# Kernel tuning notes

Measured on AMD Instinct MI355X. Metric: run time of the kernel, lower is better.

Reference implementation:

```python
import jax, jax.numpy as jnp
import numpy as np

SCALE = 8      # scale_factor from map_to_mat_info
PATCH = 32     # up_delta - low_delta + 1 == right_delta - left_delta + 1 (uniform interior patches)


def setup_inputs() -> dict:
    key = jax.random.key(0)
    mat_h, mat_w = 160, 160
    H = (mat_h - 1) * SCALE + PATCH  # 1304: deltas (0,31,0,31) -> no border clipping
    W = (mat_w - 1) * SCALE + PATCH
    x = jax.random.normal(key, (1, 3, H, W), dtype=jnp.float32)
    rgb_weight = jnp.array([0.299, 0.587, 0.114], dtype=jnp.float32).reshape(1, 3, 1, 1)
    return {"x": x, "rgb_weight": rgb_weight, "mat_h": mat_h, "mat_w": mat_w}


def reference(x, rgb_weight, mat_h, mat_w):
    P = PATCH
    # RGB -> grayscale (convert_gray branch for in_channels == 3)
    gray = jnp.sum(x * rgb_weight, axis=1)[0]  # (H, W)
    # Gather all overlapping PxP patches at stride SCALE -> (mat_h, mat_w, P, P)
    rows = (jnp.arange(mat_h) * SCALE)[:, None] + jnp.arange(P)[None, :]  # (mat_h, P)
    cols = (jnp.arange(mat_w) * SCALE)[:, None] + jnp.arange(P)[None, :]  # (mat_w, P)
    p = gray[rows.reshape(-1)].reshape(mat_h, P, -1)              # (mat_h, P, W)
    p = p[:, :, cols.reshape(-1)].reshape(mat_h, P, mat_w, P)     # (mat_h, P, mat_w, P)
    patches = jnp.transpose(p, (0, 2, 1, 3))                      # (mat_h, mat_w, P, P)
    # torch.rfft(signal_ndim=2, onesided=False) == full 2D FFT; power = re^2 + im^2
    F = jnp.fft.fft2(patches)
    log_power = jnp.log(F.real * F.real + F.imag * F.imag + 1.0)
    # High-frequency region sums (h == w == P, static)
    lo = P // 2 - P // 4 - 1   # 7
    up = P // 2 + P // 4       # 24
    r1 = jnp.sum(log_power[..., lo:up + 1, :], axis=(-2, -1))
    r2 = jnp.sum(log_power[..., up + 1:, lo:up + 1], axis=(-2, -1))
    r3 = jnp.sum(log_power[..., :lo, lo:up + 1], axis=(-2, -1))
    mat = (r1 + r2 + r3)[None, None]  # (1, 1, mat_h, mat_w)
    return mat / jnp.max(mat)
```

## Files before the change

kernel.cpp:

```cpp
#include <hip/hip_runtime.h>
#include <math.h>

#define SCALE 8
#define PSZ 32

__device__ constexpr float C32[16] = {
     1.000000000000000f,  0.980785280403230f,  0.923879532511287f,  0.831469612302545f,
     0.707106781186548f,  0.555570233019602f,  0.382683432365090f,  0.195090322016128f,
     0.000000000000000f, -0.195090322016128f, -0.382683432365090f, -0.555570233019602f,
    -0.707106781186548f, -0.831469612302545f, -0.923879532511287f, -0.980785280403230f };
__device__ constexpr float S32[16] = {
     0.000000000000000f,  0.195090322016128f,  0.382683432365090f,  0.555570233019602f,
     0.707106781186548f,  0.831469612302545f,  0.923879532511287f,  0.980785280403230f,
     1.000000000000000f,  0.980785280403230f,  0.923879532511287f,  0.831469612302545f,
     0.707106781186548f,  0.555570233019602f,  0.382683432365090f,  0.195090322016128f };

__device__ __forceinline__ constexpr int brev4(int i) {
    return ((i & 1) << 3) | ((i & 2) << 1) | ((i & 4) >> 1) | ((i & 8) >> 3);
}

__device__ __forceinline__ void fft16(float re[16], float im[16]) {
#pragma unroll
    for (int i = 0; i < 16; ++i) {
        const int j = brev4(i);
        if (j > i) {
            float t = re[i]; re[i] = re[j]; re[j] = t;
            t = im[i]; im[i] = im[j]; im[j] = t;
        }
    }
#pragma unroll
    for (int s = 1; s <= 4; ++s) {
        const int m = 1 << s;
        const int h = m >> 1;
        const int tstep = 32 >> s;
#pragma unroll
        for (int k = 0; k < 16; k += m) {
#pragma unroll
            for (int j = 0; j < h; ++j) {
                const float wr = C32[j * tstep];
                const float wi = -S32[j * tstep];
                const int a = k + j;
                const int b = k + j + h;
                const float tr = wr * re[b] - wi * im[b];
                const float ti = wr * im[b] + wi * re[b];
                re[b] = re[a] - tr; im[b] = im[a] - ti;
                re[a] = re[a] + tr; im[a] = im[a] + ti;
            }
        }
    }
}

__device__ __forceinline__ unsigned pack_bf2(float hi, float lo) {
    const unsigned uh = __float_as_uint(hi) + 0x8000u;
    const unsigned ul = __float_as_uint(lo) + 0x8000u;
    return (uh & 0xFFFF0000u) | (ul >> 16);
}
__device__ __forceinline__ float bf_hi(unsigned u) { return __uint_as_float(u & 0xFFFF0000u); }
__device__ __forceinline__ float bf_lo(unsigned u) { return __uint_as_float(u << 16); }

__global__ __launch_bounds__(256) void gray_kernel(
        const float* __restrict__ x, const float* __restrict__ w,
        float* __restrict__ g, int n4, long long HW) {
    const int i = blockIdx.x * 256 + threadIdx.x;
    if (i >= n4) return;
    const float w0 = w[0], w1 = w[1], w2 = w[2];
    const float4 a = reinterpret_cast<const float4*>(x)[i];
    const float4 b = reinterpret_cast<const float4*>(x + HW)[i];
    const float4 c = reinterpret_cast<const float4*>(x + 2 * HW)[i];
    float4 o;
    o.x = w0 * a.x + w1 * b.x + w2 * c.x;
    o.y = w0 * a.y + w1 * b.y + w2 * c.y;
    o.z = w0 * a.z + w1 * b.z + w2 * c.z;
    o.w = w0 * a.w + w1 * b.w + w2 * c.w;
    reinterpret_cast<float4*>(g)[i] = o;
}

template <bool GRAY_PRE>
__global__ __launch_bounds__(128) void hfdft_patch_kernel(
        const float* __restrict__ x, const float* __restrict__ w,
        float* __restrict__ out, int H, int W, int mat_h, int mat_w) {
    __shared__ unsigned cb[4 * 528];
    __shared__ float red[8];

    const int tid = threadIdx.x;
    const int h = tid >> 6;
    const int lane = tid & 63;
    const int total = mat_h * mat_w;
    const long long HW = (long long)H * W;
    const int Pbase = blockIdx.x * 4;

    {
        const int g = lane >> 5, r = lane & 31;
        int pA = Pbase + 2 * g;
        if (pA > total - 1) pA = total - 1;
        int pB = pA + 1; if (pB > total - 1) pB = total - 1;
        const int phA = pA / mat_w, pwA = pA % mat_w;
        const int phB = pB / mat_w, pwB = pB % mat_w;
        const bool adj = (phA == phB) && (pwB == pwA + 1);
        const int baseA = (phA * SCALE + r) * W + pwA * SCALE;
        const int baseB = (phB * SCALE + r) * W + pwB * SCALE;

        float ar[32], br[32];
        if (GRAY_PRE && adj) {
            float win[40];
            const float4* g4 = reinterpret_cast<const float4*>(x + baseA);
#pragma unroll
            for (int q = 0; q < 10; ++q) {
                const float4 v = g4[q];
                win[4 * q + 0] = v.x; win[4 * q + 1] = v.y;
                win[4 * q + 2] = v.z; win[4 * q + 3] = v.w;
            }
#pragma unroll
            for (int i = 0; i < 32; ++i) { ar[i] = win[i]; br[i] = win[i + 8]; }
        } else if (GRAY_PRE) {
#pragma unroll
            for (int i = 0; i < 32; ++i) { ar[i] = x[baseA + i]; br[i] = x[baseB + i]; }
        } else {
            const float w0 = w[0], w1 = w[1], w2 = w[2];
#pragma unroll
            for (int i = 0; i < 32; ++i) {
                ar[i] = w0 * x[baseA + i] + w1 * x[HW + baseA + i] + w2 * x[2 * HW + baseA + i];
                br[i] = w0 * x[baseB + i] + w1 * x[HW + baseB + i] + w2 * x[2 * HW + baseB + i];
            }
        }

        float fr[16], fi[16];
        if (h == 0) {
#pragma unroll
            for (int i = 0; i < 16; ++i) {
                fr[i] = ar[i] + ar[i + 16];
                fi[i] = br[i] + br[i + 16];
            }
        } else {
#pragma unroll
            for (int i = 0; i < 16; ++i) {
                const float dre = ar[i] - ar[i + 16];
                const float dim = br[i] - br[i + 16];
                fr[i] = dre * C32[i] + dim * S32[i];
                fi[i] = dim * C32[i] - dre * S32[i];
            }
        }

        fft16(fr, fi);

        unsigned* cbA = cb + (2 * g) * 528;
        unsigned* cbB = cbA + 528;
        if (h == 0) {
            cbA[r] = pack_bf2(fr[0], fr[8]);
            cbB[r] = pack_bf2(fi[0], fi[8]);
#pragma unroll
            for (int k2 = 1; k2 <= 7; ++k2) {
                const int e2 = 16 - k2;
                const float far_ = 0.5f * (fr[k2] + fr[e2]);
                const float fai_ = 0.5f * (fi[k2] - fi[e2]);
                const float fbr_ = 0.5f * (fi[k2] + fi[e2]);
                const float fbi_ = 0.5f * (fr[e2] - fr[k2]);
                cbA[(2 * k2) * 33 + r] = pack_bf2(far_, fai_);
                cbB[(2 * k2) * 33 + r] = pack_bf2(fbr_, fbi_);
            }
        } else {
#pragma unroll
            for (int k2 = 0; k2 <= 7; ++k2) {
                const int o2 = 15 - k2;
                const float far_ = 0.5f * (fr[k2] + fr[o2]);
                const float fai_ = 0.5f * (fi[k2] - fi[o2]);
                const float fbr_ = 0.5f * (fi[k2] + fi[o2]);
                const float fbi_ = 0.5f * (fr[o2] - fr[k2]);
                cbA[(2 * k2 + 1) * 33 + r] = pack_bf2(far_, fai_);
                cbB[(2 * k2 + 1) * 33 + r] = pack_bf2(fbr_, fbi_);
            }
        }
    }

    __syncthreads();

    {
        const int pl = lane >> 4, slot = lane & 15;
        int p = Pbase + pl;
        if (p > total - 1) p = total - 1;
        const unsigned* cbp = cb + pl * 528 + slot * 33;

        float fr[16], fi[16];
        if (h == 0) {
#pragma unroll
            for (int i = 0; i < 16; ++i) {
                const unsigned u0 = cbp[i], u1 = cbp[i + 16];
                fr[i] = bf_hi(u0) + bf_hi(u1);
                fi[i] = bf_lo(u0) + bf_lo(u1);
            }
        } else {
#pragma unroll
            for (int i = 0; i < 16; ++i) {
                const unsigned u0 = cbp[i], u1 = cbp[i + 16];
                const float dre = bf_hi(u0) - bf_hi(u1);
                const float dim = bf_lo(u0) - bf_lo(u1);
                fr[i] = dre * C32[i] + dim * S32[i];
                fi[i] = dim * C32[i] - dre * S32[i];
            }
        }

        fft16(fr, fi);

        float s0 = 0.0f, s1 = 0.0f;
        if (slot == 0) {
            if (h == 0) {
#pragma unroll
                for (int k2 = 0; k2 <= 8; ++k2) {
                    const int kr = 2 * k2;
                    const int b = (k2 == 0) ? 0 : 16 - k2;
                    const float g0r = 0.5f * (fr[k2] + fr[b]);
                    const float g0i = 0.5f * (fi[k2] - fi[b]);
                    const float g1r = 0.5f * (fi[k2] + fi[b]);
                    const float g1i = 0.5f * (fr[b] - fr[k2]);
                    const float w0c = (kr >= 7 ? 1.0f : 0.0f) + ((kr >= 8 && kr <= 15) ? 1.0f : 0.0f);
                    const float w16c = 1.0f + ((kr >= 1 && kr <= 15) ? 1.0f : 0.0f);
                    if (w0c > 0.0f)
                        s0 = fmaf(w0c, __logf(g0r * g0r + g0i * g0i + 1.0f), s0);
                    s1 = fmaf(w16c, __logf(g1r * g1r + g1i * g1i + 1.0f), s1);
                }
            } else {
#pragma unroll
                for (int k2 = 0; k2 <= 7; ++k2) {
                    const int kr = 2 * k2 + 1;
                    const int b = 15 - k2;
                    const float g0r = 0.5f * (fr[k2] + fr[b]);
                    const float g0i = 0.5f * (fi[k2] - fi[b]);
                    const float g1r = 0.5f * (fi[k2] + fi[b]);
                    const float g1i = 0.5f * (fr[b] - fr[k2]);
                    const float w0c = (kr >= 7 ? 1.0f : 0.0f) + ((kr >= 8 && kr <= 15) ? 1.0f : 0.0f);
                    const float w16c = 2.0f;
                    if (w0c > 0.0f)
                        s0 = fmaf(w0c, __logf(g0r * g0r + g0i * g0i + 1.0f), s0);
                    s1 = fmaf(w16c, __logf(g1r * g1r + g1i * g1i + 1.0f), s1);
                }
            }
        } else {
            const float b1f = (slot >= 7) ? 1.0f : 0.0f;
            const float m1f = (slot >= 8) ? 1.0f : 0.0f;
            if (h == 0) {
#pragma unroll
                for (int k2 = 0; k2 < 16; ++k2) {
                    const int kr = 2 * k2;
                    const float lp = __logf(fr[k2] * fr[k2] + fi[k2] * fi[k2] + 1.0f);
                    const float wgt = (kr >= 8 && kr <= 24) ? 2.0f : (b1f + m1f);
                    if (k2 & 1) s1 = fmaf(wgt, lp, s1);
                    else        s0 = fmaf(wgt, lp, s0);
                }
            } else {
#pragma unroll
                for (int k2 = 0; k2 < 16; ++k2) {
                    const int kr = 2 * k2 + 1;
                    const float lp = __logf(fr[k2] * fr[k2] + fi[k2] * fi[k2] + 1.0f);
                    float wgt;
                    if (kr == 7)                   wgt = 1.0f + m1f;
                    else if (kr == 25)             wgt = b1f + 1.0f;
                    else if (kr >= 9 && kr <= 23)  wgt = 2.0f;
                    else                           wgt = b1f + m1f;
                    if (k2 & 1) s1 = fmaf(wgt, lp, s1);
                    else        s0 = fmaf(wgt, lp, s0);
                }
            }
        }

        float s = s0 + s1;
#pragma unroll
        for (int off = 8; off >= 1; off >>= 1) s += __shfl_xor(s, off, 16);
        if (slot == 0) red[pl * 2 + h] = s;
    }

    __syncthreads();

    if (tid < 4) {
        const int p = Pbase + tid;
        if (p < total) out[p] = red[tid * 2] + red[tid * 2 + 1];
    }
}

__global__ __launch_bounds__(1024) void max_kernel(
        const float* __restrict__ sums, int n, float* __restrict__ partial) {
    __shared__ float sm[16];
    float m = 0.0f;
    for (int i = blockIdx.x * 1024 + threadIdx.x; i < n; i += gridDim.x * 1024)
        m = fmaxf(m, sums[i]);
#pragma unroll
    for (int off = 32; off >= 1; off >>= 1) m = fmaxf(m, __shfl_xor(m, off, 64));
    if ((threadIdx.x & 63) == 0) sm[threadIdx.x >> 6] = m;
    __syncthreads();
    if (threadIdx.x == 0) {
#pragma unroll
        for (int i = 1; i < 16; ++i) m = fmaxf(m, sm[i]);
        partial[blockIdx.x] = m;
    }
}

__global__ __launch_bounds__(256) void norm_kernel(
        float* __restrict__ out, int n, const float* __restrict__ partial) {
    const int i = blockIdx.x * 256 + threadIdx.x;
    float m = partial[0];
#pragma unroll
    for (int b = 1; b < 8; ++b) m = fmaxf(m, partial[b]);
    if (i < n) out[i] = out[i] / m;
}

extern "C" void kernel_launch(void* const* d_in, const int* in_sizes, int n_in,
                              void* d_out, int out_size, void* d_ws, size_t ws_size,
                              hipStream_t stream) {
    const float* x = (const float*)d_in[0];
    const float* w = (const float*)d_in[1];
    float* out = (float*)d_out;

    const int HWi = in_sizes[0] / 3;
    const int H = (int)(sqrt((double)HWi) + 0.5);
    const int W = H;
    const long long HW = (long long)H * W;
    const int mat = (int)(sqrt((double)out_size) + 0.5);
    const int total = mat * mat;
    const int blocksA = (total + 3) / 4;

    float* partial = (float*)d_ws;
    float* gray = (float*)((char*)d_ws + 256);
    const size_t need = 256 + (size_t)HW * 4;

    if (ws_size >= need && (W & 3) == 0) {
        const int n4 = (int)(HW / 4);
        hipLaunchKernelGGL(gray_kernel, dim3((n4 + 255) / 256), dim3(256), 0, stream,
                           x, w, gray, n4, HW);
        hipLaunchKernelGGL((hfdft_patch_kernel<true>), dim3(blocksA), dim3(128), 0, stream,
                           gray, w, out, H, W, mat, mat);
    } else {
        hipLaunchKernelGGL((hfdft_patch_kernel<false>), dim3(blocksA), dim3(128), 0, stream,
                           x, w, out, H, W, mat, mat);
    }
    hipLaunchKernelGGL(max_kernel, dim3(8), dim3(1024), 0, stream, out, total, partial);
    hipLaunchKernelGGL(norm_kernel, dim3((total + 255) / 256), dim3(256), 0, stream,
                       out, total, partial);
}
```

Measured before the change: 47.90 us.

## Add tiled FFT kernel sharing row DFTs across horizontally adjacent patches

Adds a tile kernel in which each block covers an 8x2 group of patches. Each of 88 threads computes the row FFT for its image row once, for two column strips, and stores half-spectra in shared memory as packed bf16. Column FFTs then read those shared row spectra, so rows shared by vertically overlapping patches are not transformed again. Real-input symmetry and the weighted region masks are applied directly, so each log-power term is computed once. This replaces the per-patch redundant row transforms, at the cost of bf16 precision in intermediates and only 88 of 256 threads active during the row phase.

```diff
diff --git a/kernel.cpp b/kernel.cpp
--- a/kernel.cpp
+++ b/kernel.cpp
@@ -75,6 +75,183 @@
     reinterpret_cast<float4*>(g)[i] = o;
 }
 
+__global__ __launch_bounds__(256) void hfdft_tile_kernel(
+        const float* __restrict__ g, float* __restrict__ out,
+        int W, int mat_w) {
+    __shared__ unsigned spec[2 * 88 * 17];
+
+    const int tid = threadIdx.x;
+    const int row0 = blockIdx.y * 64;
+    const int col0 = blockIdx.x * 16;
+
+    if (tid < 88) {
+        const int y = tid;
+        const float4* g4 = reinterpret_cast<const float4*>(
+            g + (size_t)(row0 + y) * W + col0);
+        unsigned* sA = spec + y * 17;
+        unsigned* sB = spec + 88 * 17 + y * 17;
+
+        {
+            float win[40];
+#pragma unroll
+            for (int q = 0; q < 10; ++q) {
+                const float4 v = g4[q];
+                win[4 * q + 0] = v.x; win[4 * q + 1] = v.y;
+                win[4 * q + 2] = v.z; win[4 * q + 3] = v.w;
+            }
+            float er[16], ei[16];
+#pragma unroll
+            for (int i = 0; i < 16; ++i) {
+                er[i] = win[i] + win[i + 16];
+                ei[i] = win[i + 8] + win[i + 24];
+            }
+            fft16(er, ei);
+            sA[0] = pack_bf2(er[0], er[8]);
+            sB[0] = pack_bf2(ei[0], ei[8]);
+#pragma unroll
+            for (int k2 = 1; k2 <= 7; ++k2) {
+                const int e2 = 16 - k2;
+                const float far_ = 0.5f * (er[k2] + er[e2]);
+                const float fai_ = 0.5f * (ei[k2] - ei[e2]);
+                const float fbr_ = 0.5f * (ei[k2] + ei[e2]);
+                const float fbi_ = 0.5f * (er[e2] - er[k2]);
+                sA[2 * k2] = pack_bf2(far_, fai_);
+                sB[2 * k2] = pack_bf2(fbr_, fbi_);
+            }
+        }
+
+        asm volatile("" ::: "memory");
+
+        {
+            float win[40];
+#pragma unroll
+            for (int q = 0; q < 10; ++q) {
+                const float4 v = g4[q];
+                win[4 * q + 0] = v.x; win[4 * q + 1] = v.y;
+                win[4 * q + 2] = v.z; win[4 * q + 3] = v.w;
+            }
+            float orr[16], oi[16];
+#pragma unroll
+            for (int i = 0; i < 16; ++i) {
+                const float dre = win[i] - win[i + 16];
+                const float dim = win[i + 8] - win[i + 24];
+                orr[i] = dre * C32[i] + dim * S32[i];
+                oi[i]  = dim * C32[i] - dre * S32[i];
+            }
+            fft16(orr, oi);
+#pragma unroll
+            for (int k2 = 0; k2 <= 7; ++k2) {
+                const int o2 = 15 - k2;
+                const float far_ = 0.5f * (orr[k2] + orr[o2]);
+                const float fai_ = 0.5f * (oi[k2] - oi[o2]);
+                const float fbr_ = 0.5f * (oi[k2] + oi[o2]);
+                const float fbi_ = 0.5f * (orr[o2] - orr[k2]);
+                sA[2 * k2 + 1] = pack_bf2(far_, fai_);
+                sB[2 * k2 + 1] = pack_bf2(fbr_, fbi_);
+            }
+        }
+    }
+
+    __syncthreads();
+
+    {
+        const int pl = tid >> 4;
+        const int slot = tid & 15;
+        const int ph = pl >> 1, strip = pl & 1;
+        const unsigned* cbp = spec + strip * (88 * 17) + (ph * 8) * 17 + slot;
+        const float b1f = (slot >= 7) ? 1.0f : 0.0f;
+        const float m1f = (slot >= 8) ? 1.0f : 0.0f;
+
+        float s0 = 0.0f, s1 = 0.0f;
+
+        {
+            float er[16], ei[16];
+#pragma unroll
+            for (int i = 0; i < 16; ++i) {
+                const unsigned u0 = cbp[i * 17], u1 = cbp[(i + 16) * 17];
+                er[i] = bf_hi(u0) + bf_hi(u1);
+                ei[i] = bf_lo(u0) + bf_lo(u1);
+            }
+            fft16(er, ei);
+            if (slot == 0) {
+#pragma unroll
+                for (int k2 = 0; k2 <= 8; ++k2) {
+                    const int kr = 2 * k2;
+                    const int b = (k2 == 0) ? 0 : 16 - k2;
+                    const float g0r = 0.5f * (er[k2] + er[b]);
+                    const float g0i = 0.5f * (ei[k2] - ei[b]);
+                    const float g1r = 0.5f * (ei[k2] + ei[b]);
+                    const float g1i = 0.5f * (er[b] - er[k2]);
+                    const float w0c = (kr >= 7 ? 1.0f : 0.0f) + ((kr >= 8 && kr <= 15) ? 1.0f : 0.0f);
+                    const float w16c = 1.0f + ((kr >= 1 && kr <= 15) ? 1.0f : 0.0f);
+                    if (w0c > 0.0f)
+                        s0 = fmaf(w0c, __logf(g0r * g0r + g0i * g0i + 1.0f), s0);
+                    s1 = fmaf(w16c, __logf(g1r * g1r + g1i * g1i + 1.0f), s1);
+                }
+            } else {
+#pragma unroll
+                for (int k2 = 0; k2 < 16; ++k2) {
+                    const int kr = 2 * k2;
+                    const float lp = __logf(er[k2] * er[k2] + ei[k2] * ei[k2] + 1.0f);
+                    const float wgt = (kr >= 8 && kr <= 24) ? 2.0f : (b1f + m1f);
+                    if (k2 & 1) s1 = fmaf(wgt, lp, s1);
+                    else        s0 = fmaf(wgt, lp, s0);
+                }
+            }
+        }
+
+        asm volatile("" ::: "memory");
+
+        {
+            float orr[16], oi[16];
+#pragma unroll
+            for (int i = 0; i < 16; ++i) {
+                const unsigned u0 = cbp[i * 17], u1 = cbp[(i + 16) * 17];
+                const float dre = bf_hi(u0) - bf_hi(u1);
+                const float dim = bf_lo(u0) - bf_lo(u1);
+                orr[i] = dre * C32[i] + dim * S32[i];
+                oi[i]  = dim * C32[i] - dre * S32[i];
+            }
+            fft16(orr, oi);
+            if (slot == 0) {
+#pragma unroll
+                for (int k2 = 0; k2 <= 7; ++k2) {
+                    const int kr = 2 * k2 + 1;
+                    const int b = 15 - k2;
+                    const float g0r = 0.5f * (orr[k2] + orr[b]);
+                    const float g0i = 0.5f * (oi[k2] - oi[b]);
+                    const float g1r = 0.5f * (oi[k2] + oi[b]);
+                    const float g1i = 0.5f * (orr[b] - orr[k2]);
+                    const float w0c = (kr >= 7 ? 1.0f : 0.0f) + ((kr >= 8 && kr <= 15) ? 1.0f : 0.0f);
+                    const float w16c = 2.0f;
+                    if (w0c > 0.0f)
+                        s0 = fmaf(w0c, __logf(g0r * g0r + g0i * g0i + 1.0f), s0);
+                    s1 = fmaf(w16c, __logf(g1r * g1r + g1i * g1i + 1.0f), s1);
+                }
+            } else {
+#pragma unroll
+                for (int k2 = 0; k2 < 16; ++k2) {
+                    const int kr = 2 * k2 + 1;
+                    const float lp = __logf(orr[k2] * orr[k2] + oi[k2] * oi[k2] + 1.0f);
+                    float wgt;
+                    if (kr == 7)                   wgt = 1.0f + m1f;
+                    else if (kr == 25)             wgt = b1f + 1.0f;
+                    else if (kr >= 9 && kr <= 23)  wgt = 2.0f;
+                    else                           wgt = b1f + m1f;
+                    if (k2 & 1) s1 = fmaf(wgt, lp, s1);
+                    else        s0 = fmaf(wgt, lp, s0);
+                }
+            }
+        }
+
+        float s = s0 + s1;
+#pragma unroll
+        for (int off = 8; off >= 1; off >>= 1) s += __shfl_xor(s, off, 16);
+        if (slot == 0)
+            out[(blockIdx.y * 8 + ph) * mat_w + blockIdx.x * 2 + strip] = s;
+    }
+}
+
 template <bool GRAY_PRE>
 __global__ __launch_bounds__(128) void hfdft_patch_kernel(
         const float* __restrict__ x, const float* __restrict__ w,
@@ -315,20 +492,29 @@
     const long long HW = (long long)H * W;
     const int mat = (int)(sqrt((double)out_size) + 0.5);
     const int total = mat * mat;
-    const int blocksA = (total + 3) / 4;
 
     float* partial = (float*)d_ws;
     float* gray = (float*)((char*)d_ws + 256);
     const size_t need = 256 + (size_t)HW * 4;
 
-    if (ws_size >= need && (W & 3) == 0) {
+    const bool shape_ok = ((mat & 7) == 0) && (W == (mat - 1) * SCALE + PSZ)
+                          && (H == W) && ((W & 3) == 0);
+
+    if (shape_ok && ws_size >= need) {
         const int n4 = (int)(HW / 4);
         hipLaunchKernelGGL(gray_kernel, dim3((n4 + 255) / 256), dim3(256), 0, stream,
                            x, w, gray, n4, HW);
-        hipLaunchKernelGGL((hfdft_patch_kernel<true>), dim3(blocksA), dim3(128), 0, stream,
+        dim3 gridT(mat / 2, mat / 8);
+        hipLaunchKernelGGL(hfdft_tile_kernel, gridT, dim3(256), 0, stream,
+                           gray, out, W, mat);
+    } else if (ws_size >= need && (W & 3) == 0) {
+        const int n4 = (int)(HW / 4);
+        hipLaunchKernelGGL(gray_kernel, dim3((n4 + 255) / 256), dim3(256), 0, stream,
+                           x, w, gray, n4, HW);
+        hipLaunchKernelGGL((hfdft_patch_kernel<true>), dim3((total + 3) / 4), dim3(128), 0, stream,
                            gray, w, out, H, W, mat, mat);
     } else {
-        hipLaunchKernelGGL((hfdft_patch_kernel<false>), dim3(blocksA), dim3(128), 0, stream,
+        hipLaunchKernelGGL((hfdft_patch_kernel<false>), dim3((total + 3) / 4), dim3(128), 0, stream,
                            x, w, out, H, W, mat, mat);
     }
     hipLaunchKernelGGL(max_kernel, dim3(8), dim3(1024), 0, stream, out, total, partial);
```

New measurement: 43.65 us. 1.1x faster.
